# Optimization experiments

Measured on AMD Instinct MI355X. Metric: run time of the kernel, lower is better.

Reference implementation:

```python
import jax, jax.numpy as jnp
import numpy as np
import math

IMAGE_SIZE = 512
N_ANGLES = 180
BATCH = 4


def _shepp_logan_filter(size):
    # Matches _get_fourier_filter(size, 'shepp-logan') in the torch module.
    n = np.concatenate([np.arange(1, size // 2 + 1, 2), np.arange(size // 2 - 1, 0, -2)])
    f = np.zeros(size, dtype=np.float64)
    f[0] = 0.25
    f[1::2] = -1.0 / (np.pi * n) ** 2
    ff = 2.0 * np.real(np.fft.fft(f))
    omega = np.pi * np.fft.fftfreq(size)[1:]
    ff[1:] *= np.sin(omega) / omega
    return jnp.asarray(ff, dtype=jnp.float32)


def setup_inputs() -> dict:
    key = jax.random.key(0)
    sinogram = jax.random.normal(key, (BATCH, N_ANGLES, IMAGE_SIZE), dtype=jnp.float32)
    return {"sinogram": sinogram}


def _inverse_radon(sinogram):
    B, A, P = sinogram.shape
    S = P  # image_size == proj_size (required by the torch filter expand)
    # --- FFT ramp filtering (pad_size == P for power-of-two P >= 64, so pad_width = 0) ---
    ff = _shepp_logan_filter(P)  # [P]
    filtered = jnp.real(
        jnp.fft.ifft(jnp.fft.fft(sinogram, axis=-1) * ff, axis=-1)
    ).astype(sinogram.dtype)  # [B, A, P]

    # --- backprojection grid (note: x axis is reversed, as in the torch meshgrid) ---
    x = jnp.arange(S - 1, -1, -1, dtype=jnp.float32) - S // 2  # [W]
    y = jnp.arange(S, dtype=jnp.float32) - S // 2              # [H]
    angles_rad = jnp.linspace(0.0, 180.0, A) * (math.pi / 180.0)  # [A]
    half = P // 2

    def body(acc, inp):
        theta, row = inp  # theta scalar, row: [B, P] filtered projection for this angle
        # unnormalized sample position; equals grid_sample(align_corners=True) coord
        p = x[None, :] * jnp.sin(theta) + y[:, None] * jnp.cos(theta) + half  # [H, W]
        i0f = jnp.floor(p)
        frac = p - i0f  # [H, W]
        i0 = i0f.astype(jnp.int32)
        i1 = i0 + 1

        def tap(idx):
            # bilinear tap with zeros padding (out-of-range taps contribute 0)
            valid = (idx >= 0) & (idx <= P - 1)  # [H, W]
            v = jnp.take(row, jnp.clip(idx, 0, P - 1), axis=1)  # [B, H, W]
            return jnp.where(valid[None], v, jnp.zeros((), dtype=row.dtype))

        contrib = (1.0 - frac)[None] * tap(i0) + frac[None] * tap(i1)  # [B, H, W]
        return acc + contrib, None

    out0 = jnp.zeros((B, S, S), dtype=sinogram.dtype)
    out, _ = jax.lax.scan(body, out0, (angles_rad, jnp.swapaxes(filtered, 0, 1)))
    out = out * (math.pi / (2.0 * A))

    # circle mask
    radius = S // 2
    mask = (x[None, :] ** 2 + y[:, None] ** 2) <= radius ** 2  # [H, W]
    out = out * mask[None].astype(out.dtype)
    return out[:, None]  # [B, 1, S, S]


def reference(sinogram):
    return _inverse_radon(sinogram)
```

## Files before the change

kernel.cpp:

```cpp
#include <hip/hip_runtime.h>
#include <math.h>

#define P      512
#define NA     180
#define NB     4
#define FS2    1056
#define FOFF2  16
#define GUARD  512
#define TS     32
#define WSF    100

#if __has_builtin(__builtin_amdgcn_fractf)
#define FRACT(x) __builtin_amdgcn_fractf(x)
#else
#define FRACT(x) ((x) - floorf(x))
#endif

typedef float f4g __attribute__((ext_vector_type(4), aligned(16)));
typedef float f4l __attribute__((ext_vector_type(4), aligned(8)));

__global__ __launch_bounds__(64) void ir_spectrum(float* __restrict__ ffg) {
    const int o = blockIdx.x;
    const int t = threadIdx.x;
    double s = 0.0;
    #pragma unroll
    for (int i = 0; i < 4; ++i) {
        const int m = t + 64 * i;
        const int idx = 2 * m + 1;
        const int n = (idx < 256) ? idx : (512 - idx);
        const double fv = -1.0 / ((M_PI * n) * (M_PI * n));
        const int ph = (o * idx) & 511;
        s += fv * cos((2.0 * M_PI / 512.0) * (double)ph);
    }
    #pragma unroll
    for (int off = 32; off; off >>= 1) s += __shfl_down(s, off, 64);
    if (t == 0) {
        double ff = 0.5 + 2.0 * s;
        if (o > 0) {
            const double freq = (o <= 256) ? (double)o / 512.0 : ((double)o - 512.0) / 512.0;
            const double w = M_PI * freq;
            ff *= sin(w) / w;
        }
        ffg[o] = (float)ff;
    }
}

__global__ __launch_bounds__(64) void ir_impulse(const float* __restrict__ ffg,
                                                 float* __restrict__ hr) {
    const int o = blockIdx.x;
    const int t = threadIdx.x;
    double s = 0.0;
    #pragma unroll
    for (int i = 0; i < 8; ++i) {
        const int k = t + 64 * i;
        const int ph = (o * k) & 511;
        s += (double)ffg[k] * cos((2.0 * M_PI / 512.0) * (double)ph);
    }
    #pragma unroll
    for (int off = 32; off; off >>= 1) s += __shfl_down(s, off, 64);
    if (t == 0) hr[o] = (float)(s / 512.0);
}

__global__ __launch_bounds__(256) void ir_filter(const float* __restrict__ sino,
                                                 const float* __restrict__ hr,
                                                 float* __restrict__ fil2) {
    __shared__ float row2[2][2 * P];
    const int a = blockIdx.x;
    const int p = blockIdx.y;
    const int t = threadIdx.x;
    const int r = t >> 7;
    const int tt = t & 127;
    const int b = 2 * p + r;

    const float* src = sino + ((size_t)b * NA + a) * P;
    const float4 v = *(const float4*)(src + 4 * tt);
    *(float4*)&row2[r][4 * tt] = v;
    *(float4*)&row2[r][4 * tt + P] = v;
    __syncthreads();

    float a0 = 0.f, a1 = 0.f, a2 = 0.f, a3 = 0.f;
    #pragma unroll 2
    for (int J = 0; J < P; J += 4) {
        const int base = P + 4 * tt - J;
        const float4 A  = *(const float4*)&row2[r][base];
        const float4 Bv = *(const float4*)&row2[r][base - 4];
        const float h0 = hr[J], h1 = hr[J + 1], h2v = hr[J + 2], h3 = hr[J + 3];
        a0 = fmaf(h0, A.x, a0); a0 = fmaf(h1, Bv.w, a0); a0 = fmaf(h2v, Bv.z, a0); a0 = fmaf(h3, Bv.y, a0);
        a1 = fmaf(h0, A.y, a1); a1 = fmaf(h1, A.x, a1); a1 = fmaf(h2v, Bv.w, a1); a1 = fmaf(h3, Bv.z, a1);
        a2 = fmaf(h0, A.z, a2); a2 = fmaf(h1, A.y, a2); a2 = fmaf(h2v, A.x, a2); a2 = fmaf(h3, Bv.w, a2);
        a3 = fmaf(h0, A.w, a3); a3 = fmaf(h1, A.z, a3); a3 = fmaf(h2v, A.y, a3); a3 = fmaf(h3, A.x, a3);
    }
    float* frow = fil2 + ((size_t)p * NA + a) * FS2;
    const int o0 = FOFF2 + 8 * tt + r;
    frow[o0]     = a0;
    frow[o0 + 2] = a1;
    frow[o0 + 4] = a2;
    frow[o0 + 6] = a3;
    if (t < FOFF2) {
        frow[t] = 0.f;
        frow[FOFF2 + 2 * P + t] = 0.f;
    }
}

__global__ __launch_bounds__(256) void ir_backproject(const float* __restrict__ fil2,
                                                      float* __restrict__ out) {
    __shared__ float4 angc[NA];
    __shared__ float win[NA * WSF];

    const int t = threadIdx.x;
    const int lane = t & 63;
    const int wave = t >> 6;
    const int w0 = blockIdx.x * TS, h0 = blockIdx.y * TS;
    const int p = blockIdx.z;

    const int w = w0 + (lane & 15);
    const int h = h0 + (lane >> 4) + 4 * wave;

    const int ix0 = 255 - w, ix1 = ix0 - 16;
    const int iy0 = h - 256, iy1 = iy0 + 16;
    const int r2 = 256 * 256;
    const int m00 = (ix0 * ix0 + iy0 * iy0) <= r2;
    const int m01 = (ix1 * ix1 + iy0 * iy0) <= r2;
    const int m10 = (ix0 * ix0 + iy1 * iy1) <= r2;
    const int m11 = (ix1 * ix1 + iy1 * iy1) <= r2;

    float* o0 = out + (((size_t)(2 * p) * P) + h) * P + w;
    float* o1 = o0 + (size_t)P * P;

    if (__syncthreads_count(m00 | m01 | m10 | m11) == 0) {
        o0[0] = 0.f; o0[16] = 0.f; o0[16 * P] = 0.f; o0[16 * P + 16] = 0.f;
        o1[0] = 0.f; o1[16] = 0.f; o1[16 * P] = 0.f; o1[16 * P + 16] = 0.f;
        return;
    }

    if (t < NA) {
        const float th = (float)t * (float)(M_PI / (double)(NA - 1));
        const float s = sinf(th), c = cosf(th);
        const float xlo = (float)(224 - w0);
        const float ylo = (float)(h0 - 256), yhi = (float)(h0 - 225);
        const float pmin = s * xlo + fminf(c * ylo, c * yhi) + 256.0f;
        const int base = ((int)floorf(pmin) - 2) & ~1;
        angc[t] = make_float4(s, c, (float)(256 - base), (float)base);
    }
    __syncthreads();

    const float* fbase = fil2 + (size_t)p * NA * FS2;
    for (int idx = t; idx < NA * (WSF / 4); idx += 256) {
        const int a = idx / (WSF / 4);
        const int i = idx - a * (WSF / 4);
        const int base = (int)angc[a].w;
        const f4g vv = *(const f4g*)(fbase + a * FS2 + FOFF2 + 2 * base + 4 * i);
        *(f4g*)(win + a * WSF + 4 * i) = vv;
    }
    __syncthreads();

    const float xf = (float)ix0;
    const float yf = (float)iy0;
    float a00 = 0.f, a01 = 0.f, a10 = 0.f, a11 = 0.f;
    float b00 = 0.f, b01 = 0.f, b10 = 0.f, b11 = 0.f;
    #pragma unroll 2
    for (int a = 0; a < NA; ++a) {
        const float4 ac = angc[a];
        const float q00 = fmaf(xf, ac.x, fmaf(yf, ac.y, ac.z));
        const float q01 = fmaf(-16.f, ac.x, q00);
        const float q10 = fmaf( 16.f, ac.y, q00);
        const float q11 = fmaf( 16.f, ac.y, q01);
        const float* wb = win + a * WSF;
        {
            const int j = (int)q00; const float fr = FRACT(q00);
            const f4l W = *(const f4l*)(wb + 2 * j);
            a00 = fmaf(1.f - fr, W.x, fmaf(fr, W.z, a00));
            b00 = fmaf(1.f - fr, W.y, fmaf(fr, W.w, b00));
        }
        {
            const int j = (int)q01; const float fr = FRACT(q01);
            const f4l W = *(const f4l*)(wb + 2 * j);
            a01 = fmaf(1.f - fr, W.x, fmaf(fr, W.z, a01));
            b01 = fmaf(1.f - fr, W.y, fmaf(fr, W.w, b01));
        }
        {
            const int j = (int)q10; const float fr = FRACT(q10);
            const f4l W = *(const f4l*)(wb + 2 * j);
            a10 = fmaf(1.f - fr, W.x, fmaf(fr, W.z, a10));
            b10 = fmaf(1.f - fr, W.y, fmaf(fr, W.w, b10));
        }
        {
            const int j = (int)q11; const float fr = FRACT(q11);
            const f4l W = *(const f4l*)(wb + 2 * j);
            a11 = fmaf(1.f - fr, W.x, fmaf(fr, W.z, a11));
            b11 = fmaf(1.f - fr, W.y, fmaf(fr, W.w, b11));
        }
    }

    const float scale = (float)(M_PI / (2.0 * NA));
    o0[0]           = m00 ? a00 * scale : 0.f;
    o0[16]          = m01 ? a01 * scale : 0.f;
    o0[16 * P]      = m10 ? a10 * scale : 0.f;
    o0[16 * P + 16] = m11 ? a11 * scale : 0.f;
    o1[0]           = m00 ? b00 * scale : 0.f;
    o1[16]          = m01 ? b01 * scale : 0.f;
    o1[16 * P]      = m10 ? b10 * scale : 0.f;
    o1[16 * P + 16] = m11 ? b11 * scale : 0.f;
}

extern "C" void kernel_launch(void* const* d_in, const int* in_sizes, int n_in,
                              void* d_out, int out_size, void* d_ws, size_t ws_size,
                              hipStream_t stream) {
    const float* sino = (const float*)d_in[0];
    float* out = (float*)d_out;
    float* ws = (float*)d_ws;

    float* ffg  = ws;
    float* hr   = ws + 512;
    float* fil2 = ws + 1024 + GUARD;

    ir_spectrum<<<P, 64, 0, stream>>>(ffg);
    ir_impulse<<<P, 64, 0, stream>>>(ffg, hr);

    dim3 gridF(NA, NB / 2);
    ir_filter<<<gridF, 256, 0, stream>>>(sino, hr, fil2);

    dim3 gridB(P / TS, P / TS, NB / 2);
    ir_backproject<<<gridB, 256, 0, stream>>>(fil2, out);
}
```

Baseline: 121.2 us.

## Stage backprojection window in two angle halves and reuse filter row loads

Result: faster. 115.1 us (-5.0%).

```diff
diff --git a/kernel.cpp b/kernel.cpp
--- a/kernel.cpp
+++ b/kernel.cpp
@@ -9,6 +9,7 @@
 #define GUARD  512
 #define TS     32
 #define WSF    100
+#define AHALF  90
 
 #if __has_builtin(__builtin_amdgcn_fractf)
 #define FRACT(x) __builtin_amdgcn_fractf(x)
@@ -78,17 +79,18 @@
     *(float4*)&row2[r][4 * tt + P] = v;
     __syncthreads();
 
+    const int base0 = P + 4 * tt;
+    float4 A = *(const float4*)&row2[r][base0];
     float a0 = 0.f, a1 = 0.f, a2 = 0.f, a3 = 0.f;
-    #pragma unroll 2
+    #pragma unroll 4
     for (int J = 0; J < P; J += 4) {
-        const int base = P + 4 * tt - J;
-        const float4 A  = *(const float4*)&row2[r][base];
-        const float4 Bv = *(const float4*)&row2[r][base - 4];
+        const float4 Bv = *(const float4*)&row2[r][base0 - J - 4];
         const float h0 = hr[J], h1 = hr[J + 1], h2v = hr[J + 2], h3 = hr[J + 3];
         a0 = fmaf(h0, A.x, a0); a0 = fmaf(h1, Bv.w, a0); a0 = fmaf(h2v, Bv.z, a0); a0 = fmaf(h3, Bv.y, a0);
         a1 = fmaf(h0, A.y, a1); a1 = fmaf(h1, A.x, a1); a1 = fmaf(h2v, Bv.w, a1); a1 = fmaf(h3, Bv.z, a1);
         a2 = fmaf(h0, A.z, a2); a2 = fmaf(h1, A.y, a2); a2 = fmaf(h2v, A.x, a2); a2 = fmaf(h3, Bv.w, a2);
         a3 = fmaf(h0, A.w, a3); a3 = fmaf(h1, A.z, a3); a3 = fmaf(h2v, A.y, a3); a3 = fmaf(h3, A.x, a3);
+        A = Bv;
     }
     float* frow = fil2 + ((size_t)p * NA + a) * FS2;
     const int o0 = FOFF2 + 8 * tt + r;
@@ -105,7 +107,7 @@
 __global__ __launch_bounds__(256) void ir_backproject(const float* __restrict__ fil2,
                                                       float* __restrict__ out) {
     __shared__ float4 angc[NA];
-    __shared__ float win[NA * WSF];
+    __shared__ float win[AHALF * WSF];
 
     const int t = threadIdx.x;
     const int lane = t & 63;
@@ -144,52 +146,60 @@
     }
     __syncthreads();
 
-    const float* fbase = fil2 + (size_t)p * NA * FS2;
-    for (int idx = t; idx < NA * (WSF / 4); idx += 256) {
-        const int a = idx / (WSF / 4);
-        const int i = idx - a * (WSF / 4);
-        const int base = (int)angc[a].w;
-        const f4g vv = *(const f4g*)(fbase + a * FS2 + FOFF2 + 2 * base + 4 * i);
-        *(f4g*)(win + a * WSF + 4 * i) = vv;
-    }
-    __syncthreads();
-
     const float xf = (float)ix0;
     const float yf = (float)iy0;
+    const float* fbase = fil2 + (size_t)p * NA * FS2;
     float a00 = 0.f, a01 = 0.f, a10 = 0.f, a11 = 0.f;
     float b00 = 0.f, b01 = 0.f, b10 = 0.f, b11 = 0.f;
-    #pragma unroll 2
-    for (int a = 0; a < NA; ++a) {
-        const float4 ac = angc[a];
-        const float q00 = fmaf(xf, ac.x, fmaf(yf, ac.y, ac.z));
-        const float q01 = fmaf(-16.f, ac.x, q00);
-        const float q10 = fmaf( 16.f, ac.y, q00);
-        const float q11 = fmaf( 16.f, ac.y, q01);
-        const float* wb = win + a * WSF;
-        {
-            const int j = (int)q00; const float fr = FRACT(q00);
-            const f4l W = *(const f4l*)(wb + 2 * j);
-            a00 = fmaf(1.f - fr, W.x, fmaf(fr, W.z, a00));
-            b00 = fmaf(1.f - fr, W.y, fmaf(fr, W.w, b00));
+
+    #pragma unroll
+    for (int half = 0; half < 2; ++half) {
+        const int A0 = half * AHALF;
+
+        for (int idx = t; idx < AHALF * (WSF / 4); idx += 256) {
+            const int al = idx / (WSF / 4);
+            const int i = idx - al * (WSF / 4);
+            const int a = A0 + al;
+            const int base = (int)angc[a].w;
+            const f4g vv = *(const f4g*)(fbase + a * FS2 + FOFF2 + 2 * base + 4 * i);
+            *(f4g*)(win + al * WSF + 4 * i) = vv;
         }
-        {
-            const int j = (int)q01; const float fr = FRACT(q01);
-            const f4l W = *(const f4l*)(wb + 2 * j);
-            a01 = fmaf(1.f - fr, W.x, fmaf(fr, W.z, a01));
-            b01 = fmaf(1.f - fr, W.y, fmaf(fr, W.w, b01));
+        __syncthreads();
+
+        #pragma unroll 2
+        for (int al = 0; al < AHALF; ++al) {
+            const float4 ac = angc[A0 + al];
+            const float q00 = fmaf(xf, ac.x, fmaf(yf, ac.y, ac.z));
+            const float q01 = fmaf(-16.f, ac.x, q00);
+            const float q10 = fmaf( 16.f, ac.y, q00);
+            const float q11 = fmaf( 16.f, ac.y, q01);
+            const float* wb = win + al * WSF;
+            {
+                const int j = (int)q00; const float fr = FRACT(q00);
+                const f4l W = *(const f4l*)(wb + 2 * j);
+                a00 = fmaf(1.f - fr, W.x, fmaf(fr, W.z, a00));
+                b00 = fmaf(1.f - fr, W.y, fmaf(fr, W.w, b00));
+            }
+            {
+                const int j = (int)q01; const float fr = FRACT(q01);
+                const f4l W = *(const f4l*)(wb + 2 * j);
+                a01 = fmaf(1.f - fr, W.x, fmaf(fr, W.z, a01));
+                b01 = fmaf(1.f - fr, W.y, fmaf(fr, W.w, b01));
+            }
+            {
+                const int j = (int)q10; const float fr = FRACT(q10);
+                const f4l W = *(const f4l*)(wb + 2 * j);
+                a10 = fmaf(1.f - fr, W.x, fmaf(fr, W.z, a10));
+                b10 = fmaf(1.f - fr, W.y, fmaf(fr, W.w, b10));
+            }
+            {
+                const int j = (int)q11; const float fr = FRACT(q11);
+                const f4l W = *(const f4l*)(wb + 2 * j);
+                a11 = fmaf(1.f - fr, W.x, fmaf(fr, W.z, a11));
+                b11 = fmaf(1.f - fr, W.y, fmaf(fr, W.w, b11));
+            }
         }
-        {
-            const int j = (int)q10; const float fr = FRACT(q10);
-            const f4l W = *(const f4l*)(wb + 2 * j);
-            a10 = fmaf(1.f - fr, W.x, fmaf(fr, W.z, a10));
-            b10 = fmaf(1.f - fr, W.y, fmaf(fr, W.w, b10));
-        }
-        {
-            const int j = (int)q11; const float fr = FRACT(q11);
-            const f4l W = *(const f4l*)(wb + 2 * j);
-            a11 = fmaf(1.f - fr, W.x, fmaf(fr, W.z, a11));
-            b11 = fmaf(1.f - fr, W.y, fmaf(fr, W.w, b11));
-        }
+        if (half == 0) __syncthreads();
     }
 
     const float scale = (float)(M_PI / (2.0 * NA));
```
